# Kernel tuning notes

Measured on AMD Instinct MI355X. Metric: run time of the kernel, lower is better.

Reference implementation:

```python
import jax, jax.numpy as jnp
import numpy as np

N_NODES = 50000
N_EDGES = 1600000
D_IN = 256
HEADS = 4
SUB_IN = 64   # generate_sub_head_nums(256, 4) -> [64, 64, 64, 64]
SUB_H = 64    # hidden_dim // head_num


def setup_inputs() -> dict:
    key = jax.random.key(0)
    k1, k2, k3 = jax.random.split(key, 3)
    x = jax.random.normal(k1, (N_NODES, D_IN), dtype=jnp.float32)
    edge_index = jax.random.randint(k2, (2, N_EDGES), 0, N_NODES, dtype=jnp.int64)
    # per-head GCNConv weights: glorot-ish scale
    W = jax.random.normal(k3, (HEADS, SUB_IN, SUB_H), dtype=jnp.float32) * (1.0 / np.sqrt(SUB_IN))
    b = jnp.zeros((HEADS, SUB_H), dtype=jnp.float32)
    return {"x": x, "edge_index": edge_index, "W": W, "b": b}


def _gcn_aggregate(x_sub, edge_index, n_nodes):
    """Symmetric-normalized aggregation with self-loops: D^-1/2 (A+I) D^-1/2 x_sub."""
    row, col = edge_index[0], edge_index[1]          # source -> target
    loops = jnp.arange(n_nodes, dtype=row.dtype)
    row2 = jnp.concatenate([row, loops])
    col2 = jnp.concatenate([col, loops])
    deg = jax.ops.segment_sum(jnp.ones_like(col2, dtype=x_sub.dtype), col2,
                              num_segments=n_nodes)
    dinv = jnp.where(deg > 0, jax.lax.rsqrt(deg), 0.0)
    norm = dinv[row2] * dinv[col2]                   # [E+N]
    msgs = x_sub[row2] * norm[:, None]               # [E+N, SUB_IN] gather
    return jax.ops.segment_sum(msgs, col2, num_segments=n_nodes)  # [N, SUB_IN] scatter


def reference(x, edge_index, W, b):
    n = x.shape[0]
    # Faithful to source bug: `start` never advances, so every head reads x[:, 0:SUB_IN].
    x0 = x[:, :SUB_IN]                               # [N, 64], shared by all heads
    # aggregation is linear -> aggregate once, then apply per-head linear (same math as GCNConv(xW))
    agg = _gcn_aggregate(x0, edge_index, n)          # [N, 64]
    heads = jax.nn.relu(jnp.einsum('nf,hfo->nho', agg, W) + b[None, :, :])  # [N, H, SUB_H]
    x_cat = heads.reshape(n, HEADS * SUB_H)          # concat over heads along last dim
    return x_cat, heads
```

## Files before the change

### kernel.cpp

```cpp
#include <hip/hip_runtime.h>
#include <hip/hip_bf16.h>

#define NNODES 50000
#define NEDGES 1600000
#define NBIN   782
#define CAPB   2880
#define SCAP   512
#define OVFCAP 65536
#define BCHUNK 2000
#define NBBLK  800

__device__ __forceinline__ float bf2f(unsigned short u) {
    union { unsigned int i; float f; } x; x.i = ((unsigned int)u) << 16; return x.f;
}

__global__ __launch_bounds__(256) void k_bin(const int* __restrict__ edges,
                                             int* __restrict__ bincur,
                                             int* __restrict__ ovfcnt,
                                             int* __restrict__ ovf,
                                             int* __restrict__ binned) {
    __shared__ int pk[BCHUNK];
    __shared__ int hist[NBIN];
    __shared__ int gbase[NBIN];
    __shared__ int lcnt[NBIN];
    int t = threadIdx.x;
    int e0 = blockIdx.x * BCHUNK;
    unsigned xcd;
    asm volatile("s_getreg_b32 %0, hwreg(HW_REG_XCC_ID)" : "=s"(xcd));
    xcd &= 7;
    for (int i = t; i < NBIN; i += 256) { hist[i] = 0; lcnt[i] = 0; }
    __syncthreads();
    for (int i = t * 4; i < BCHUNK; i += 1024) {
        int4 r4 = *(const int4*)&edges[e0 + i];
        int4 c4 = *(const int4*)&edges[NEDGES + e0 + i];
        int b0 = c4.x >> 6, b1 = c4.y >> 6, b2 = c4.z >> 6, b3 = c4.w >> 6;
        pk[i + 0] = r4.x | ((c4.x & 63) << 16) | (b0 << 22);
        pk[i + 1] = r4.y | ((c4.y & 63) << 16) | (b1 << 22);
        pk[i + 2] = r4.z | ((c4.z & 63) << 16) | (b2 << 22);
        pk[i + 3] = r4.w | ((c4.w & 63) << 16) | (b3 << 22);
        atomicAdd(&hist[b0], 1);
        atomicAdd(&hist[b1], 1);
        atomicAdd(&hist[b2], 1);
        atomicAdd(&hist[b3], 1);
    }
    __syncthreads();
    for (int i = t; i < NBIN; i += 256) {
        int h = hist[i];
        gbase[i] = (h > 0) ? atomicAdd(&bincur[xcd * NBIN + i], h) : 0;
    }
    __syncthreads();
    for (int i = t; i < BCHUNK; i += 256) {
        int v = pk[i];
        int bin = ((unsigned)v) >> 22;
        int p = gbase[bin] + atomicAdd(&lcnt[bin], 1);
        if (p < SCAP) {
            binned[(xcd * NBIN + bin) * SCAP + p] = v & 0x3FFFFF;
        } else {
            int op = atomicAdd(ovfcnt, 1);
            if (op < OVFCAP) ovf[op] = v;
        }
    }
}

__global__ __launch_bounds__(256) void k_sortbin(const int* __restrict__ bincur,
                                                 const int* __restrict__ binned,
                                                 const int* __restrict__ ovfcnt,
                                                 const int* __restrict__ ovf,
                                                 const float* __restrict__ x,
                                                 int* __restrict__ rowptr,
                                                 int* __restrict__ cntn,
                                                 float* __restrict__ dinv,
                                                 unsigned short* __restrict__ x0s,
                                                 int* __restrict__ csr) {
    __shared__ int h[64];
    __shared__ int off[64];
    __shared__ int cur[64];
    __shared__ float dv[64];
    __shared__ int slen[8];
    __shared__ int stage[CAPB];
    int t = threadIdx.x, bin = blockIdx.x;
    int wave = t >> 6, lane = t & 63;
    if (t < 64) h[t] = 0;
    if (t < 8) slen[t] = min(bincur[t * NBIN + bin], SCAP);
    __syncthreads();
    int novf = ovfcnt[0];
    for (int s = 0; s < 8; ++s) {
        const int* __restrict__ bb = binned + (s * NBIN + bin) * SCAP;
        int len = slen[s];
        for (int e = t; e < len; e += 256)
            atomicAdd(&h[bb[e] >> 16], 1);
    }
    for (int e = t; e < novf; e += 256) {
        int v = ovf[e];
        if (((unsigned)v >> 22) == (unsigned)bin) atomicAdd(&h[(v >> 16) & 63], 1);
    }
    __syncthreads();
    if (t < 64) {
        int v = h[t];
        int inc = v;
        #pragma unroll
        for (int d = 1; d < 64; d <<= 1) {
            int u = __shfl_up(inc, d);
            if (lane >= d) inc += u;
        }
        int ex = inc - v;
        off[t] = ex;
        cur[t] = ex;
        float dc = rsqrtf((float)(v + 1));
        dv[t] = dc;
        int n = bin * 64 + t;
        if (n < NNODES) {
            dinv[n] = dc;
            rowptr[n] = bin * CAPB + ex;
            cntn[n] = v;
        }
    }
    __syncthreads();
    for (int s = 0; s < 8; ++s) {
        const int* __restrict__ bb = binned + (s * NBIN + bin) * SCAP;
        int len = slen[s];
        for (int e = t; e < len; e += 256) {
            int v = bb[e];
            int p = atomicAdd(&cur[v >> 16], 1);
            if (p < CAPB) stage[p] = v & 0xFFFF;
        }
    }
    for (int e = t; e < novf; e += 256) {
        int v = ovf[e];
        if (((unsigned)v >> 22) == (unsigned)bin) {
            int p = atomicAdd(&cur[(v >> 16) & 63], 1);
            if (p < CAPB) stage[p] = v & 0xFFFF;
        }
    }
    __syncthreads();
    int total = min(off[63] + h[63], CAPB);
    for (int e = t; e < total; e += 256)
        csr[bin * CAPB + e] = stage[e];
    for (int i = wave; i < 64; i += 4) {
        int n = bin * 64 + i;
        if (n < NNODES) {
            __hip_bfloat16 v = __float2bfloat16(x[n * 256 + lane] * dv[i]);
            x0s[n * 64 + lane] = *(unsigned short*)&v;
        }
    }
}

__global__ __launch_bounds__(256) void k_gather(const unsigned short* __restrict__ x0s,
                                                const int* __restrict__ rowptr,
                                                const int* __restrict__ cntn,
                                                const float* __restrict__ dinv,
                                                const int* __restrict__ csr,
                                                float* __restrict__ agg) {
    int wave = threadIdx.x >> 6, lane = threadIdx.x & 63;
    int n = blockIdx.x * 4 + wave;
    int start = rowptr[n], len = cntn[n];
    float acc0 = bf2f(x0s[n * 64 + lane]);
    float acc1 = 0.0f;
    for (int base = 0; base < len; base += 64) {
        int m = min(len - base, 64);
        int idx = (lane < m) ? csr[start + base + lane] : 0;
        int j = 0;
        for (; j + 8 <= m; j += 8) {
            int r0 = __shfl(idx, j + 0), r1 = __shfl(idx, j + 1);
            int r2 = __shfl(idx, j + 2), r3 = __shfl(idx, j + 3);
            int r4 = __shfl(idx, j + 4), r5 = __shfl(idx, j + 5);
            int r6 = __shfl(idx, j + 6), r7 = __shfl(idx, j + 7);
            float f0 = bf2f(x0s[r0 * 64 + lane]);
            float f1 = bf2f(x0s[r1 * 64 + lane]);
            float f2 = bf2f(x0s[r2 * 64 + lane]);
            float f3 = bf2f(x0s[r3 * 64 + lane]);
            float f4 = bf2f(x0s[r4 * 64 + lane]);
            float f5 = bf2f(x0s[r5 * 64 + lane]);
            float f6 = bf2f(x0s[r6 * 64 + lane]);
            float f7 = bf2f(x0s[r7 * 64 + lane]);
            acc0 += (f0 + f1) + (f2 + f3);
            acc1 += (f4 + f5) + (f6 + f7);
        }
        for (; j < m; ++j) {
            int r = __shfl(idx, j);
            acc0 += bf2f(x0s[r * 64 + lane]);
        }
    }
    agg[n * 64 + lane] = (acc0 + acc1) * dinv[n];
}

__global__ __launch_bounds__(256) void k_gemm(const float* __restrict__ agg,
                                              const float* __restrict__ W,
                                              const float* __restrict__ b,
                                              float* __restrict__ out0,
                                              float* __restrict__ out1) {
    int t = threadIdx.x;
    int h = t >> 6, o = t & 63;
    float wreg[64];
    #pragma unroll
    for (int f = 0; f < 64; ++f) wreg[f] = W[h * 4096 + f * 64 + o];
    float bias = b[t];
    int n0 = blockIdx.x * 8;
    for (int i = 0; i < 8; ++i) {
        int n = n0 + i;
        const float* __restrict__ arow = agg + n * 64;
        float acc = bias;
        #pragma unroll
        for (int f = 0; f < 64; ++f) acc = fmaf(arow[f], wreg[f], acc);
        float v = fmaxf(acc, 0.0f);
        __builtin_nontemporal_store(v, &out0[n * 256 + t]);
        __builtin_nontemporal_store(v, &out1[n * 256 + t]);
    }
}


extern "C" void kernel_launch(void* const* d_in, const int* in_sizes, int n_in,
                              void* d_out, int out_size, void* d_ws, size_t ws_size,
                              hipStream_t stream) {
    const float* x     = (const float*)d_in[0];
    const int*   edges = (const int*)d_in[1];
    const float* W     = (const float*)d_in[2];
    const float* b     = (const float*)d_in[3];

    float* out0 = (float*)d_out;
    float* out1 = out0 + (size_t)NNODES * 256;

    char* ws = (char*)d_ws;
    int*            bincur = (int*)(ws + 0);
    int*            ovfcnt = (int*)(ws + 25024);
    int*            ovf    = (int*)(ws + 25600);
    float*          dinv   = (float*)(ws + 287744);
    int*            rowptr = (int*)(ws + 487936);
    int*            cntn   = (int*)(ws + 688128);
    int*            binned = (int*)(ws + 888320);
    int*            csr    = (int*)(ws + 13700608);
    unsigned short* x0s    = (unsigned short*)(ws + 22709248);
    float*          agg    = (float*)(ws + 29109248);

    hipMemsetAsync(ws, 0, 25028, stream);
    k_bin    <<<NBBLK, 256, 0, stream>>>(edges, bincur, ovfcnt, ovf, binned);
    k_sortbin<<<NBIN, 256, 0, stream>>>(bincur, binned, ovfcnt, ovf, x, rowptr, cntn, dinv, x0s, csr);
    k_gather <<<NNODES / 4, 256, 0, stream>>>(x0s, rowptr, cntn, dinv, csr, agg);
    k_gemm   <<<NNODES / 8, 256, 0, stream>>>(agg, W, b, out0, out1);
}
```

Baseline: 245.6 us.

## Replace CSR build and gather with per-bin LDS atomic aggregation fused with GEMM

Drops the per-bin CSR sort (staging, prefix scan, csr write) and the separate gather and GEMM kernels. A new per-bin kernel accumulates neighbor features into a 64x64 LDS tile using shared-memory float atomics straight from the binned edge lists, then scales by dinv and applies the per-head linear layer plus ReLU from LDS. This removes the csr and agg round trips through global memory and two launches. In exchange it adds LDS atomic contention, gives each bin only 782 blocks of parallelism for the gather, and makes every block scan the whole overflow list.

```diff
diff --git a/kernel.cpp b/kernel.cpp
--- a/kernel.cpp
+++ b/kernel.cpp
@@ -4,7 +4,6 @@
 #define NNODES 50000
 #define NEDGES 1600000
 #define NBIN   782
-#define CAPB   2880
 #define SCAP   512
 #define OVFCAP 65536
 #define BCHUNK 2000
@@ -62,80 +61,38 @@
     }
 }
 
-__global__ __launch_bounds__(256) void k_sortbin(const int* __restrict__ bincur,
-                                                 const int* __restrict__ binned,
-                                                 const int* __restrict__ ovfcnt,
-                                                 const int* __restrict__ ovf,
-                                                 const float* __restrict__ x,
-                                                 int* __restrict__ rowptr,
-                                                 int* __restrict__ cntn,
-                                                 float* __restrict__ dinv,
-                                                 unsigned short* __restrict__ x0s,
-                                                 int* __restrict__ csr) {
+__global__ __launch_bounds__(256) void k_prep(const int* __restrict__ bincur,
+                                              const int* __restrict__ binned,
+                                              const int* __restrict__ ovfcnt,
+                                              const int* __restrict__ ovf,
+                                              const float* __restrict__ x,
+                                              float* __restrict__ dinv,
+                                              unsigned short* __restrict__ x0s) {
     __shared__ int h[64];
-    __shared__ int off[64];
-    __shared__ int cur[64];
     __shared__ float dv[64];
-    __shared__ int slen[8];
-    __shared__ int stage[CAPB];
     int t = threadIdx.x, bin = blockIdx.x;
     int wave = t >> 6, lane = t & 63;
     if (t < 64) h[t] = 0;
-    if (t < 8) slen[t] = min(bincur[t * NBIN + bin], SCAP);
-    __syncthreads();
+    __syncthreads();
+    for (int s = 0; s < 8; ++s) {
+        int len = min(bincur[s * NBIN + bin], SCAP);
+        const int* __restrict__ bb = binned + (s * NBIN + bin) * SCAP;
+        for (int e = t; e < len; e += 256)
+            atomicAdd(&h[(bb[e] >> 16) & 63], 1);
+    }
     int novf = ovfcnt[0];
-    for (int s = 0; s < 8; ++s) {
-        const int* __restrict__ bb = binned + (s * NBIN + bin) * SCAP;
-        int len = slen[s];
-        for (int e = t; e < len; e += 256)
-            atomicAdd(&h[bb[e] >> 16], 1);
-    }
     for (int e = t; e < novf; e += 256) {
         int v = ovf[e];
         if (((unsigned)v >> 22) == (unsigned)bin) atomicAdd(&h[(v >> 16) & 63], 1);
     }
     __syncthreads();
     if (t < 64) {
-        int v = h[t];
-        int inc = v;
-        #pragma unroll
-        for (int d = 1; d < 64; d <<= 1) {
-            int u = __shfl_up(inc, d);
-            if (lane >= d) inc += u;
-        }
-        int ex = inc - v;
-        off[t] = ex;
-        cur[t] = ex;
-        float dc = rsqrtf((float)(v + 1));
+        float dc = rsqrtf((float)(h[t] + 1));
         dv[t] = dc;
         int n = bin * 64 + t;
-        if (n < NNODES) {
-            dinv[n] = dc;
-            rowptr[n] = bin * CAPB + ex;
-            cntn[n] = v;
-        }
-    }
-    __syncthreads();
-    for (int s = 0; s < 8; ++s) {
-        const int* __restrict__ bb = binned + (s * NBIN + bin) * SCAP;
-        int len = slen[s];
-        for (int e = t; e < len; e += 256) {
-            int v = bb[e];
-            int p = atomicAdd(&cur[v >> 16], 1);
-            if (p < CAPB) stage[p] = v & 0xFFFF;
-        }
-    }
-    for (int e = t; e < novf; e += 256) {
-        int v = ovf[e];
-        if (((unsigned)v >> 22) == (unsigned)bin) {
-            int p = atomicAdd(&cur[(v >> 16) & 63], 1);
-            if (p < CAPB) stage[p] = v & 0xFFFF;
-        }
-    }
-    __syncthreads();
-    int total = min(off[63] + h[63], CAPB);
-    for (int e = t; e < total; e += 256)
-        csr[bin * CAPB + e] = stage[e];
+        if (n < NNODES) dinv[n] = dc;
+    }
+    __syncthreads();
     for (int i = wave; i < 64; i += 4) {
         int n = bin * 64 + i;
         if (n < NNODES) {
@@ -145,66 +102,100 @@
     }
 }
 
-__global__ __launch_bounds__(256) void k_gather(const unsigned short* __restrict__ x0s,
-                                                const int* __restrict__ rowptr,
-                                                const int* __restrict__ cntn,
-                                                const float* __restrict__ dinv,
-                                                const int* __restrict__ csr,
-                                                float* __restrict__ agg) {
-    int wave = threadIdx.x >> 6, lane = threadIdx.x & 63;
-    int n = blockIdx.x * 4 + wave;
-    int start = rowptr[n], len = cntn[n];
-    float acc0 = bf2f(x0s[n * 64 + lane]);
-    float acc1 = 0.0f;
-    for (int base = 0; base < len; base += 64) {
-        int m = min(len - base, 64);
-        int idx = (lane < m) ? csr[start + base + lane] : 0;
-        int j = 0;
-        for (; j + 8 <= m; j += 8) {
-            int r0 = __shfl(idx, j + 0), r1 = __shfl(idx, j + 1);
-            int r2 = __shfl(idx, j + 2), r3 = __shfl(idx, j + 3);
-            int r4 = __shfl(idx, j + 4), r5 = __shfl(idx, j + 5);
-            int r6 = __shfl(idx, j + 6), r7 = __shfl(idx, j + 7);
-            float f0 = bf2f(x0s[r0 * 64 + lane]);
-            float f1 = bf2f(x0s[r1 * 64 + lane]);
-            float f2 = bf2f(x0s[r2 * 64 + lane]);
-            float f3 = bf2f(x0s[r3 * 64 + lane]);
-            float f4 = bf2f(x0s[r4 * 64 + lane]);
-            float f5 = bf2f(x0s[r5 * 64 + lane]);
-            float f6 = bf2f(x0s[r6 * 64 + lane]);
-            float f7 = bf2f(x0s[r7 * 64 + lane]);
-            acc0 += (f0 + f1) + (f2 + f3);
-            acc1 += (f4 + f5) + (f6 + f7);
-        }
-        for (; j < m; ++j) {
-            int r = __shfl(idx, j);
-            acc0 += bf2f(x0s[r * 64 + lane]);
-        }
-    }
-    agg[n * 64 + lane] = (acc0 + acc1) * dinv[n];
-}
-
-__global__ __launch_bounds__(256) void k_gemm(const float* __restrict__ agg,
-                                              const float* __restrict__ W,
-                                              const float* __restrict__ b,
-                                              float* __restrict__ out0,
-                                              float* __restrict__ out1) {
-    int t = threadIdx.x;
-    int h = t >> 6, o = t & 63;
+__global__ __launch_bounds__(256) void k_agg(const int* __restrict__ bincur,
+                                             const int* __restrict__ binned,
+                                             const int* __restrict__ ovfcnt,
+                                             const int* __restrict__ ovf,
+                                             const unsigned short* __restrict__ x0s,
+                                             const float* __restrict__ dinv,
+                                             const float* __restrict__ W,
+                                             const float* __restrict__ b,
+                                             float* __restrict__ out0,
+                                             float* __restrict__ out1) {
+    __shared__ float acc[64 * 64];
+    int t = threadIdx.x, bin = blockIdx.x;
+    int wave = t >> 6, lane = t & 63;
+    int n0 = bin * 64;
+    for (int i = wave; i < 64; i += 4) {
+        int n = n0 + i;
+        acc[i * 64 + lane] = (n < NNODES) ? bf2f(x0s[n * 64 + lane]) : 0.0f;
+    }
+    __syncthreads();
+    for (int s = 0; s < 8; ++s) {
+        int len = min(bincur[s * NBIN + bin], SCAP);
+        const int* __restrict__ bb = binned + (s * NBIN + bin) * SCAP;
+        for (int base = wave * 64; base < len; base += 256) {
+            int m = min(len - base, 64);
+            int v = (lane < m) ? bb[base + lane] : 0;
+            int j = 0;
+            for (; j + 8 <= m; j += 8) {
+                int v0 = __shfl(v, j + 0), v1 = __shfl(v, j + 1);
+                int v2 = __shfl(v, j + 2), v3 = __shfl(v, j + 3);
+                int v4 = __shfl(v, j + 4), v5 = __shfl(v, j + 5);
+                int v6 = __shfl(v, j + 6), v7 = __shfl(v, j + 7);
+                float f0 = bf2f(x0s[(v0 & 0xFFFF) * 64 + lane]);
+                float f1 = bf2f(x0s[(v1 & 0xFFFF) * 64 + lane]);
+                float f2 = bf2f(x0s[(v2 & 0xFFFF) * 64 + lane]);
+                float f3 = bf2f(x0s[(v3 & 0xFFFF) * 64 + lane]);
+                float f4 = bf2f(x0s[(v4 & 0xFFFF) * 64 + lane]);
+                float f5 = bf2f(x0s[(v5 & 0xFFFF) * 64 + lane]);
+                float f6 = bf2f(x0s[(v6 & 0xFFFF) * 64 + lane]);
+                float f7 = bf2f(x0s[(v7 & 0xFFFF) * 64 + lane]);
+                atomicAdd(&acc[((v0 >> 16) & 63) * 64 + lane], f0);
+                atomicAdd(&acc[((v1 >> 16) & 63) * 64 + lane], f1);
+                atomicAdd(&acc[((v2 >> 16) & 63) * 64 + lane], f2);
+                atomicAdd(&acc[((v3 >> 16) & 63) * 64 + lane], f3);
+                atomicAdd(&acc[((v4 >> 16) & 63) * 64 + lane], f4);
+                atomicAdd(&acc[((v5 >> 16) & 63) * 64 + lane], f5);
+                atomicAdd(&acc[((v6 >> 16) & 63) * 64 + lane], f6);
+                atomicAdd(&acc[((v7 >> 16) & 63) * 64 + lane], f7);
+            }
+            for (; j < m; ++j) {
+                int vv = __shfl(v, j);
+                float f = bf2f(x0s[(vv & 0xFFFF) * 64 + lane]);
+                atomicAdd(&acc[((vv >> 16) & 63) * 64 + lane], f);
+            }
+        }
+    }
+    int novf = ovfcnt[0];
+    for (int base = wave * 64; base < novf; base += 256) {
+        int m = min(novf - base, 64);
+        int v = (lane < m) ? ovf[base + lane] : 0;
+        for (int j = 0; j < m; ++j) {
+            int vv = __shfl(v, j);
+            if (((unsigned)vv >> 22) == (unsigned)bin) {
+                float f = bf2f(x0s[(vv & 0xFFFF) * 64 + lane]);
+                atomicAdd(&acc[((vv >> 16) & 63) * 64 + lane], f);
+            }
+        }
+    }
+    __syncthreads();
+    for (int i = wave; i < 64; i += 4) {
+        int n = n0 + i;
+        float dc = (n < NNODES) ? dinv[n] : 0.0f;
+        acc[i * 64 + lane] *= dc;
+    }
+    __syncthreads();
     float wreg[64];
     #pragma unroll
-    for (int f = 0; f < 64; ++f) wreg[f] = W[h * 4096 + f * 64 + o];
+    for (int f = 0; f < 64; ++f) wreg[f] = W[wave * 4096 + f * 64 + lane];
     float bias = b[t];
-    int n0 = blockIdx.x * 8;
-    for (int i = 0; i < 8; ++i) {
+    int nmax = min(64, NNODES - n0);
+    for (int i = 0; i < nmax; ++i) {
+        const float4* __restrict__ av = (const float4*)&acc[i * 64];
+        float s0 = bias, s1 = 0.0f, s2 = 0.0f, s3 = 0.0f;
+        #pragma unroll
+        for (int f4 = 0; f4 < 16; ++f4) {
+            float4 a = av[f4];
+            s0 = fmaf(a.x, wreg[4 * f4 + 0], s0);
+            s1 = fmaf(a.y, wreg[4 * f4 + 1], s1);
+            s2 = fmaf(a.z, wreg[4 * f4 + 2], s2);
+            s3 = fmaf(a.w, wreg[4 * f4 + 3], s3);
+        }
+        float vv = fmaxf((s0 + s1) + (s2 + s3), 0.0f);
         int n = n0 + i;
-        const float* __restrict__ arow = agg + n * 64;
-        float acc = bias;
-        #pragma unroll
-        for (int f = 0; f < 64; ++f) acc = fmaf(arow[f], wreg[f], acc);
-        float v = fmaxf(acc, 0.0f);
-        __builtin_nontemporal_store(v, &out0[n * 256 + t]);
-        __builtin_nontemporal_store(v, &out1[n * 256 + t]);
+        __builtin_nontemporal_store(vv, &out0[n * 256 + t]);
+        __builtin_nontemporal_store(vv, &out1[n * 256 + t]);
     }
 }
 
@@ -225,16 +216,11 @@
     int*            ovfcnt = (int*)(ws + 25024);
     int*            ovf    = (int*)(ws + 25600);
     float*          dinv   = (float*)(ws + 287744);
-    int*            rowptr = (int*)(ws + 487936);
-    int*            cntn   = (int*)(ws + 688128);
-    int*            binned = (int*)(ws + 888320);
-    int*            csr    = (int*)(ws + 13700608);
-    unsigned short* x0s    = (unsigned short*)(ws + 22709248);
-    float*          agg    = (float*)(ws + 29109248);
+    unsigned short* x0s    = (unsigned short*)(ws + 488448);
+    int*            binned = (int*)(ws + 6888448);
 
     hipMemsetAsync(ws, 0, 25028, stream);
-    k_bin    <<<NBBLK, 256, 0, stream>>>(edges, bincur, ovfcnt, ovf, binned);
-    k_sortbin<<<NBIN, 256, 0, stream>>>(bincur, binned, ovfcnt, ovf, x, rowptr, cntn, dinv, x0s, csr);
-    k_gather <<<NNODES / 4, 256, 0, stream>>>(x0s, rowptr, cntn, dinv, csr, agg);
-    k_gemm   <<<NNODES / 8, 256, 0, stream>>>(agg, W, b, out0, out1);
-}
+    k_bin <<<NBBLK, 256, 0, stream>>>(edges, bincur, ovfcnt, ovf, binned);
+    k_prep<<<NBIN, 256, 0, stream>>>(bincur, binned, ovfcnt, ovf, x, dinv, x0s);
+    k_agg <<<NBIN, 256, 0, stream>>>(bincur, binned, ovfcnt, ovf, x0s, dinv, W, b, out0, out1);
+}
```

New measurement: 924.4 us. 3.76x slower.

## Replace per-bin CSR sort with per-XCD per-node slot lists and degree counters

Applied to the files above, without the earlier changes.

Per-node degree is now counted with global atomics per XCD partition during binning. The single per-bin sort kernel is split into a node-wise prep kernel (degree, dinv, bf16 scaled features) and a segment kernel. The segment kernel writes edges into fixed 20-slot per-node lists for each XCD partition, with a global overflow list. The gather kernel walks the eight sublists and then scans the overflow list for its node. This aims to spread the sort work across more blocks and remove the large shared staging buffer. In exchange it adds many global atomics, a larger memset, and a per-wave linear overflow scan that could be costly if overflow is nonempty.

```diff
diff --git a/kernel.cpp b/kernel.cpp
--- a/kernel.cpp
+++ b/kernel.cpp
@@ -4,8 +4,8 @@
 #define NNODES 50000
 #define NEDGES 1600000
 #define NBIN   782
-#define CAPB   2880
 #define SCAP   512
+#define SCAPN  20
 #define OVFCAP 65536
 #define BCHUNK 2000
 #define NBBLK  800
@@ -16,6 +16,7 @@
 
 __global__ __launch_bounds__(256) void k_bin(const int* __restrict__ edges,
                                              int* __restrict__ bincur,
+                                             int* __restrict__ curnx,
                                              int* __restrict__ ovfcnt,
                                              int* __restrict__ ovf,
                                              int* __restrict__ binned) {
@@ -55,6 +56,8 @@
         int p = gbase[bin] + atomicAdd(&lcnt[bin], 1);
         if (p < SCAP) {
             binned[(xcd * NBIN + bin) * SCAP + p] = v & 0x3FFFFF;
+            int c = (bin << 6) | ((v >> 16) & 63);
+            atomicAdd(&curnx[xcd * NNODES + c], 1);
         } else {
             int op = atomicAdd(ovfcnt, 1);
             if (op < OVFCAP) ovf[op] = v;
@@ -62,103 +65,103 @@
     }
 }
 
-__global__ __launch_bounds__(256) void k_sortbin(const int* __restrict__ bincur,
-                                                 const int* __restrict__ binned,
-                                                 const int* __restrict__ ovfcnt,
-                                                 const int* __restrict__ ovf,
-                                                 const float* __restrict__ x,
-                                                 int* __restrict__ rowptr,
-                                                 int* __restrict__ cntn,
-                                                 float* __restrict__ dinv,
-                                                 unsigned short* __restrict__ x0s,
-                                                 int* __restrict__ csr) {
-    __shared__ int h[64];
-    __shared__ int off[64];
+__global__ __launch_bounds__(256) void k_prep(const int* __restrict__ curnx,
+                                              const int* __restrict__ ovfcnt,
+                                              const int* __restrict__ ovf,
+                                              const float* __restrict__ x,
+                                              float* __restrict__ dinv,
+                                              uint2* __restrict__ cnt8,
+                                              unsigned short* __restrict__ x0s) {
+    __shared__ float dv[128];
+    int t = threadIdx.x;
+    int nb = blockIdx.x * 128;
+    if (t < 128) {
+        int n = nb + t;
+        if (n < NNODES) {
+            int c[8]; int deg = 0;
+            #pragma unroll
+            for (int s = 0; s < 8; ++s) { c[s] = curnx[s * NNODES + n]; deg += c[s]; }
+            int novf = min(ovfcnt[0], OVFCAP);
+            for (int e = 0; e < novf; ++e) {
+                int v = ovf[e];
+                int cc = ((((unsigned)v) >> 22) << 6) | ((v >> 16) & 63);
+                if (cc == n) ++deg;
+            }
+            float dc = rsqrtf((float)(deg + 1));
+            dinv[n] = dc; dv[t] = dc;
+            unsigned lo = (unsigned)min(c[0], SCAPN) | ((unsigned)min(c[1], SCAPN) << 8)
+                        | ((unsigned)min(c[2], SCAPN) << 16) | ((unsigned)min(c[3], SCAPN) << 24);
+            unsigned hi = (unsigned)min(c[4], SCAPN) | ((unsigned)min(c[5], SCAPN) << 8)
+                        | ((unsigned)min(c[6], SCAPN) << 16) | ((unsigned)min(c[7], SCAPN) << 24);
+            cnt8[n] = make_uint2(lo, hi);
+        } else dv[t] = 0.0f;
+    }
+    __syncthreads();
+    int lane = t & 63, w = t >> 6;
+    for (int i = w; i < 128; i += 4) {
+        int n = nb + i;
+        if (n < NNODES) {
+            __hip_bfloat16 bv = __float2bfloat16(x[n * 256 + lane] * dv[i]);
+            x0s[n * 64 + lane] = *(unsigned short*)&bv;
+        }
+    }
+}
+
+__global__ __launch_bounds__(256) void k_seg(const int* __restrict__ bincur,
+                                             const int* __restrict__ binned,
+                                             int* __restrict__ ovfcnt,
+                                             int* __restrict__ ovf,
+                                             int* __restrict__ csrx) {
     __shared__ int cur[64];
-    __shared__ float dv[64];
-    __shared__ int slen[8];
-    __shared__ int stage[CAPB];
-    int t = threadIdx.x, bin = blockIdx.x;
-    int wave = t >> 6, lane = t & 63;
-    if (t < 64) h[t] = 0;
-    if (t < 8) slen[t] = min(bincur[t * NBIN + bin], SCAP);
-    __syncthreads();
-    int novf = ovfcnt[0];
-    for (int s = 0; s < 8; ++s) {
-        const int* __restrict__ bb = binned + (s * NBIN + bin) * SCAP;
-        int len = slen[s];
-        for (int e = t; e < len; e += 256)
-            atomicAdd(&h[bb[e] >> 16], 1);
-    }
-    for (int e = t; e < novf; e += 256) {
-        int v = ovf[e];
-        if (((unsigned)v >> 22) == (unsigned)bin) atomicAdd(&h[(v >> 16) & 63], 1);
-    }
-    __syncthreads();
-    if (t < 64) {
-        int v = h[t];
-        int inc = v;
-        #pragma unroll
-        for (int d = 1; d < 64; d <<= 1) {
-            int u = __shfl_up(inc, d);
-            if (lane >= d) inc += u;
-        }
-        int ex = inc - v;
-        off[t] = ex;
-        cur[t] = ex;
-        float dc = rsqrtf((float)(v + 1));
-        dv[t] = dc;
-        int n = bin * 64 + t;
-        if (n < NNODES) {
-            dinv[n] = dc;
-            rowptr[n] = bin * CAPB + ex;
-            cntn[n] = v;
-        }
-    }
-    __syncthreads();
-    for (int s = 0; s < 8; ++s) {
-        const int* __restrict__ bb = binned + (s * NBIN + bin) * SCAP;
-        int len = slen[s];
-        for (int e = t; e < len; e += 256) {
-            int v = bb[e];
-            int p = atomicAdd(&cur[v >> 16], 1);
-            if (p < CAPB) stage[p] = v & 0xFFFF;
-        }
-    }
-    for (int e = t; e < novf; e += 256) {
-        int v = ovf[e];
-        if (((unsigned)v >> 22) == (unsigned)bin) {
-            int p = atomicAdd(&cur[(v >> 16) & 63], 1);
-            if (p < CAPB) stage[p] = v & 0xFFFF;
-        }
-    }
-    __syncthreads();
-    int total = min(off[63] + h[63], CAPB);
-    for (int e = t; e < total; e += 256)
-        csr[bin * CAPB + e] = stage[e];
-    for (int i = wave; i < 64; i += 4) {
-        int n = bin * 64 + i;
-        if (n < NNODES) {
-            __hip_bfloat16 v = __float2bfloat16(x[n * 256 + lane] * dv[i]);
-            x0s[n * 64 + lane] = *(unsigned short*)&v;
-        }
-    }
-}
-
-__global__ __launch_bounds__(256) void k_gather(const unsigned short* __restrict__ x0s,
-                                                const int* __restrict__ rowptr,
-                                                const int* __restrict__ cntn,
+    int t = threadIdx.x;
+    int bin = blockIdx.x >> 3, s = blockIdx.x & 7;
+    if (t < 64) cur[t] = 0;
+    __syncthreads();
+    int len = min(bincur[s * NBIN + bin], SCAP);
+    const int* __restrict__ bb = binned + (s * NBIN + bin) * SCAP;
+    for (int e = t; e < len; e += 256) {
+        int v = bb[e];
+        int c63 = (v >> 16) & 63;
+        int rank = atomicAdd(&cur[c63], 1);
+        int n = (bin << 6) | c63;
+        if (rank < SCAPN) {
+            csrx[(s * NNODES + n) * SCAPN + rank] = v & 0xFFFF;
+        } else {
+            int op = atomicAdd(ovfcnt, 1);
+            if (op < OVFCAP) ovf[op] = (v & 0x3FFFFF) | (bin << 22);
+        }
+    }
+}
+
+__global__ __launch_bounds__(256) void k_gather(const int* __restrict__ csrx,
+                                                const uint2* __restrict__ cnt8,
+                                                const int* __restrict__ ovfcnt,
+                                                const int* __restrict__ ovf,
+                                                const unsigned short* __restrict__ x0s,
                                                 const float* __restrict__ dinv,
-                                                const int* __restrict__ csr,
                                                 float* __restrict__ agg) {
-    int wave = threadIdx.x >> 6, lane = threadIdx.x & 63;
-    int n = blockIdx.x * 4 + wave;
-    int start = rowptr[n], len = cntn[n];
+    int t = threadIdx.x, lane = t & 63, w = t >> 6;
+    int n = blockIdx.x * 4 + w;
+    uint2 c8 = cnt8[n];
+    int cl[8], pre[8];
+    cl[0] = c8.x & 255; cl[1] = (c8.x >> 8) & 255; cl[2] = (c8.x >> 16) & 255; cl[3] = (c8.x >> 24) & 255;
+    cl[4] = c8.y & 255; cl[5] = (c8.y >> 8) & 255; cl[6] = (c8.y >> 16) & 255; cl[7] = (c8.y >> 24) & 255;
+    int acc = 0;
+    #pragma unroll
+    for (int s = 0; s < 8; ++s) { pre[s] = acc; acc += cl[s]; }
+    int cnt = acc;
     float acc0 = bf2f(x0s[n * 64 + lane]);
     float acc1 = 0.0f;
-    for (int base = 0; base < len; base += 64) {
-        int m = min(len - base, 64);
-        int idx = (lane < m) ? csr[start + base + lane] : 0;
+    for (int base = 0; base < cnt; base += 64) {
+        int m = min(cnt - base, 64);
+        int ti = base + lane;
+        int addr = 0;
+        #pragma unroll
+        for (int s = 0; s < 8; ++s) {
+            if (ti >= pre[s] && ti < pre[s] + cl[s])
+                addr = (s * NNODES + n) * SCAPN + (ti - pre[s]);
+        }
+        int idx = (lane < m) ? csrx[addr] : 0;
         int j = 0;
         for (; j + 8 <= m; j += 8) {
             int r0 = __shfl(idx, j + 0), r1 = __shfl(idx, j + 1);
@@ -181,6 +184,12 @@
             acc0 += bf2f(x0s[r * 64 + lane]);
         }
     }
+    int novf = min(ovfcnt[0], OVFCAP);
+    for (int e = 0; e < novf; ++e) {
+        int v = ovf[e];
+        int c = ((((unsigned)v) >> 22) << 6) | ((v >> 16) & 63);
+        if (c == n) acc0 += bf2f(x0s[(v & 0xFFFF) * 64 + lane]);
+    }
     agg[n * 64 + lane] = (acc0 + acc1) * dinv[n];
 }
 
@@ -221,20 +230,21 @@
     float* out1 = out0 + (size_t)NNODES * 256;
 
     char* ws = (char*)d_ws;
-    int*            bincur = (int*)(ws + 0);
-    int*            ovfcnt = (int*)(ws + 25024);
-    int*            ovf    = (int*)(ws + 25600);
-    float*          dinv   = (float*)(ws + 287744);
-    int*            rowptr = (int*)(ws + 487936);
-    int*            cntn   = (int*)(ws + 688128);
-    int*            binned = (int*)(ws + 888320);
-    int*            csr    = (int*)(ws + 13700608);
-    unsigned short* x0s    = (unsigned short*)(ws + 22709248);
-    float*          agg    = (float*)(ws + 29109248);
-
-    hipMemsetAsync(ws, 0, 25028, stream);
-    k_bin    <<<NBBLK, 256, 0, stream>>>(edges, bincur, ovfcnt, ovf, binned);
-    k_sortbin<<<NBIN, 256, 0, stream>>>(bincur, binned, ovfcnt, ovf, x, rowptr, cntn, dinv, x0s, csr);
-    k_gather <<<NNODES / 4, 256, 0, stream>>>(x0s, rowptr, cntn, dinv, csr, agg);
-    k_gemm   <<<NNODES / 8, 256, 0, stream>>>(agg, W, b, out0, out1);
-}
+    int*            curnx  = (int*)(ws + 0);
+    int*            bincur = (int*)(ws + 1600000);
+    int*            ovfcnt = (int*)(ws + 1625024);
+    int*            ovf    = (int*)(ws + 1625600);
+    float*          dinv   = (float*)(ws + 1887744);
+    uint2*          cnt8   = (uint2*)(ws + 2088448);
+    unsigned short* x0s    = (unsigned short*)(ws + 2488448);
+    int*            binned = (int*)(ws + 8888448);
+    int*            csrx   = (int*)(ws + 21701120);
+    float*          agg    = (float*)(ws + 53701120);
+
+    hipMemsetAsync(ws, 0, 1625028, stream);
+    k_bin   <<<NBBLK, 256, 0, stream>>>(edges, bincur, curnx, ovfcnt, ovf, binned);
+    k_prep  <<<(NNODES + 127) / 128, 256, 0, stream>>>(curnx, ovfcnt, ovf, x, dinv, cnt8, x0s);
+    k_seg   <<<NBIN * 8, 256, 0, stream>>>(bincur, binned, ovfcnt, ovf, csrx);
+    k_gather<<<NNODES / 4, 256, 0, stream>>>(csrx, cnt8, ovfcnt, ovf, x0s, dinv, agg);
+    k_gemm  <<<NNODES / 8, 256, 0, stream>>>(agg, W, b, out0, out1);
+}
```

Measured after the change: 316.1 us. 1.29x slower.

## Halve bin width to 32 nodes, prefetch x rows, enlarge GEMM node chunk

Applied to the files above, without the earlier changes.

Bins now cover 32 destination nodes instead of 64, which doubles the number of sort blocks (1564) and halves per-block staging and shared memory. The sort kernel splits its threads so two sub-bins are scanned concurrently, and it loads the x rows into registers at kernel start so their latency overlaps the histogram work. The GEMM kernel handles 25 nodes per block instead of 8, which amortises the per-block load of W into registers over more rows. The trade-offs are more per-XCD bin counters to zero and atomically update, and a smaller per-bin capacity that may push more edges onto the slow overflow path.

```diff
diff --git a/kernel.cpp b/kernel.cpp
--- a/kernel.cpp
+++ b/kernel.cpp
@@ -3,9 +3,9 @@
 
 #define NNODES 50000
 #define NEDGES 1600000
-#define NBIN   782
-#define CAPB   2880
-#define SCAP   512
+#define NBIN2  1564
+#define CAPB2  1440
+#define SCAP   320
 #define OVFCAP 65536
 #define BCHUNK 2000
 #define NBBLK  800
@@ -20,41 +20,41 @@
                                              int* __restrict__ ovf,
                                              int* __restrict__ binned) {
     __shared__ int pk[BCHUNK];
-    __shared__ int hist[NBIN];
-    __shared__ int gbase[NBIN];
-    __shared__ int lcnt[NBIN];
+    __shared__ int hist[NBIN2];
+    __shared__ int gbase[NBIN2];
+    __shared__ int lcnt[NBIN2];
     int t = threadIdx.x;
     int e0 = blockIdx.x * BCHUNK;
     unsigned xcd;
     asm volatile("s_getreg_b32 %0, hwreg(HW_REG_XCC_ID)" : "=s"(xcd));
     xcd &= 7;
-    for (int i = t; i < NBIN; i += 256) { hist[i] = 0; lcnt[i] = 0; }
+    for (int i = t; i < NBIN2; i += 256) { hist[i] = 0; lcnt[i] = 0; }
     __syncthreads();
     for (int i = t * 4; i < BCHUNK; i += 1024) {
         int4 r4 = *(const int4*)&edges[e0 + i];
         int4 c4 = *(const int4*)&edges[NEDGES + e0 + i];
-        int b0 = c4.x >> 6, b1 = c4.y >> 6, b2 = c4.z >> 6, b3 = c4.w >> 6;
-        pk[i + 0] = r4.x | ((c4.x & 63) << 16) | (b0 << 22);
-        pk[i + 1] = r4.y | ((c4.y & 63) << 16) | (b1 << 22);
-        pk[i + 2] = r4.z | ((c4.z & 63) << 16) | (b2 << 22);
-        pk[i + 3] = r4.w | ((c4.w & 63) << 16) | (b3 << 22);
+        int b0 = c4.x >> 5, b1 = c4.y >> 5, b2 = c4.z >> 5, b3 = c4.w >> 5;
+        pk[i + 0] = r4.x | ((c4.x & 31) << 16) | (b0 << 21);
+        pk[i + 1] = r4.y | ((c4.y & 31) << 16) | (b1 << 21);
+        pk[i + 2] = r4.z | ((c4.z & 31) << 16) | (b2 << 21);
+        pk[i + 3] = r4.w | ((c4.w & 31) << 16) | (b3 << 21);
         atomicAdd(&hist[b0], 1);
         atomicAdd(&hist[b1], 1);
         atomicAdd(&hist[b2], 1);
         atomicAdd(&hist[b3], 1);
     }
     __syncthreads();
-    for (int i = t; i < NBIN; i += 256) {
+    for (int i = t; i < NBIN2; i += 256) {
         int h = hist[i];
-        gbase[i] = (h > 0) ? atomicAdd(&bincur[xcd * NBIN + i], h) : 0;
+        gbase[i] = (h > 0) ? atomicAdd(&bincur[xcd * NBIN2 + i], h) : 0;
     }
     __syncthreads();
     for (int i = t; i < BCHUNK; i += 256) {
         int v = pk[i];
-        int bin = ((unsigned)v) >> 22;
+        int bin = ((unsigned)v) >> 21;
         int p = gbase[bin] + atomicAdd(&lcnt[bin], 1);
         if (p < SCAP) {
-            binned[(xcd * NBIN + bin) * SCAP + p] = v & 0x3FFFFF;
+            binned[(xcd * NBIN2 + bin) * SCAP + p] = v;
         } else {
             int op = atomicAdd(ovfcnt, 1);
             if (op < OVFCAP) ovf[op] = v;
@@ -72,34 +72,43 @@
                                                  float* __restrict__ dinv,
                                                  unsigned short* __restrict__ x0s,
                                                  int* __restrict__ csr) {
-    __shared__ int h[64];
-    __shared__ int off[64];
-    __shared__ int cur[64];
-    __shared__ float dv[64];
+    __shared__ int h[32];
+    __shared__ int off[32];
+    __shared__ int cur[32];
+    __shared__ float dv[32];
     __shared__ int slen[8];
-    __shared__ int stage[CAPB];
+    __shared__ int stage[CAPB2];
     int t = threadIdx.x, bin = blockIdx.x;
     int wave = t >> 6, lane = t & 63;
-    if (t < 64) h[t] = 0;
-    if (t < 8) slen[t] = min(bincur[t * NBIN + bin], SCAP);
+    int n0 = bin * 32;
+    float xv[8];
+    #pragma unroll
+    for (int k = 0; k < 8; ++k) {
+        int n = n0 + wave + 4 * k;
+        xv[k] = (n < NNODES) ? x[n * 256 + lane] : 0.0f;
+    }
+    if (t < 32) h[t] = 0;
+    if (t < 8) slen[t] = min(bincur[t * NBIN2 + bin], SCAP);
     __syncthreads();
     int novf = ovfcnt[0];
-    for (int s = 0; s < 8; ++s) {
-        const int* __restrict__ bb = binned + (s * NBIN + bin) * SCAP;
+    for (int sp = 0; sp < 8; sp += 2) {
+        int s = sp + (t >> 7);
+        int tl = t & 127;
         int len = slen[s];
-        for (int e = t; e < len; e += 256)
-            atomicAdd(&h[bb[e] >> 16], 1);
+        const int* __restrict__ bb = binned + (s * NBIN2 + bin) * SCAP;
+        for (int e = tl; e < len; e += 128)
+            atomicAdd(&h[(bb[e] >> 16) & 31], 1);
     }
     for (int e = t; e < novf; e += 256) {
         int v = ovf[e];
-        if (((unsigned)v >> 22) == (unsigned)bin) atomicAdd(&h[(v >> 16) & 63], 1);
-    }
-    __syncthreads();
-    if (t < 64) {
+        if (((unsigned)v >> 21) == (unsigned)bin) atomicAdd(&h[(v >> 16) & 31], 1);
+    }
+    __syncthreads();
+    if (t < 32) {
         int v = h[t];
         int inc = v;
         #pragma unroll
-        for (int d = 1; d < 64; d <<= 1) {
+        for (int d = 1; d < 32; d <<= 1) {
             int u = __shfl_up(inc, d);
             if (lane >= d) inc += u;
         }
@@ -108,38 +117,42 @@
         cur[t] = ex;
         float dc = rsqrtf((float)(v + 1));
         dv[t] = dc;
-        int n = bin * 64 + t;
+        int n = n0 + t;
         if (n < NNODES) {
             dinv[n] = dc;
-            rowptr[n] = bin * CAPB + ex;
+            rowptr[n] = bin * CAPB2 + ex;
             cntn[n] = v;
         }
     }
     __syncthreads();
-    for (int s = 0; s < 8; ++s) {
-        const int* __restrict__ bb = binned + (s * NBIN + bin) * SCAP;
+    for (int sp = 0; sp < 8; sp += 2) {
+        int s = sp + (t >> 7);
+        int tl = t & 127;
         int len = slen[s];
-        for (int e = t; e < len; e += 256) {
+        const int* __restrict__ bb = binned + (s * NBIN2 + bin) * SCAP;
+        for (int e = tl; e < len; e += 128) {
             int v = bb[e];
-            int p = atomicAdd(&cur[v >> 16], 1);
-            if (p < CAPB) stage[p] = v & 0xFFFF;
+            int p = atomicAdd(&cur[(v >> 16) & 31], 1);
+            if (p < CAPB2) stage[p] = v & 0xFFFF;
         }
     }
     for (int e = t; e < novf; e += 256) {
         int v = ovf[e];
-        if (((unsigned)v >> 22) == (unsigned)bin) {
-            int p = atomicAdd(&cur[(v >> 16) & 63], 1);
-            if (p < CAPB) stage[p] = v & 0xFFFF;
-        }
-    }
-    __syncthreads();
-    int total = min(off[63] + h[63], CAPB);
+        if (((unsigned)v >> 21) == (unsigned)bin) {
+            int p = atomicAdd(&cur[(v >> 16) & 31], 1);
+            if (p < CAPB2) stage[p] = v & 0xFFFF;
+        }
+    }
+    __syncthreads();
+    int total = min(off[31] + h[31], CAPB2);
     for (int e = t; e < total; e += 256)
-        csr[bin * CAPB + e] = stage[e];
-    for (int i = wave; i < 64; i += 4) {
-        int n = bin * 64 + i;
+        csr[bin * CAPB2 + e] = stage[e];
+    #pragma unroll
+    for (int k = 0; k < 8; ++k) {
+        int i = wave + 4 * k;
+        int n = n0 + i;
         if (n < NNODES) {
-            __hip_bfloat16 v = __float2bfloat16(x[n * 256 + lane] * dv[i]);
+            __hip_bfloat16 v = __float2bfloat16(xv[k] * dv[i]);
             x0s[n * 64 + lane] = *(unsigned short*)&v;
         }
     }
@@ -195,8 +208,8 @@
     #pragma unroll
     for (int f = 0; f < 64; ++f) wreg[f] = W[h * 4096 + f * 64 + o];
     float bias = b[t];
-    int n0 = blockIdx.x * 8;
-    for (int i = 0; i < 8; ++i) {
+    int n0 = blockIdx.x * 25;
+    for (int i = 0; i < 25; ++i) {
         int n = n0 + i;
         const float* __restrict__ arow = agg + n * 64;
         float acc = bias;
@@ -222,19 +235,19 @@
 
     char* ws = (char*)d_ws;
     int*            bincur = (int*)(ws + 0);
-    int*            ovfcnt = (int*)(ws + 25024);
-    int*            ovf    = (int*)(ws + 25600);
-    float*          dinv   = (float*)(ws + 287744);
-    int*            rowptr = (int*)(ws + 487936);
-    int*            cntn   = (int*)(ws + 688128);
-    int*            binned = (int*)(ws + 888320);
-    int*            csr    = (int*)(ws + 13700608);
-    unsigned short* x0s    = (unsigned short*)(ws + 22709248);
-    float*          agg    = (float*)(ws + 29109248);
-
-    hipMemsetAsync(ws, 0, 25028, stream);
+    int*            ovfcnt = (int*)(ws + 50176);
+    int*            ovf    = (int*)(ws + 50688);
+    float*          dinv   = (float*)(ws + 312832);
+    int*            rowptr = (int*)(ws + 513024);
+    int*            cntn   = (int*)(ws + 713216);
+    int*            binned = (int*)(ws + 913408);
+    int*            csr    = (int*)(ws + 16928768);
+    unsigned short* x0s    = (unsigned short*)(ws + 25937408);
+    float*          agg    = (float*)(ws + 32337408);
+
+    hipMemsetAsync(ws, 0, 50180, stream);
     k_bin    <<<NBBLK, 256, 0, stream>>>(edges, bincur, ovfcnt, ovf, binned);
-    k_sortbin<<<NBIN, 256, 0, stream>>>(bincur, binned, ovfcnt, ovf, x, rowptr, cntn, dinv, x0s, csr);
+    k_sortbin<<<NBIN2, 256, 0, stream>>>(bincur, binned, ovfcnt, ovf, x, rowptr, cntn, dinv, x0s, csr);
     k_gather <<<NNODES / 4, 256, 0, stream>>>(x0s, rowptr, cntn, dinv, csr, agg);
-    k_gemm   <<<NNODES / 8, 256, 0, stream>>>(agg, W, b, out0, out1);
-}
+    k_gemm   <<<2000, 256, 0, stream>>>(agg, W, b, out0, out1);
+}
```

After: 244.5 us. Within noise of the previous version (-0.4%).
